# Optimization experiments

Hardware: AMD Instinct MI355X
Metric: run time of the kernel (lower is better)

The kernel has to match this reference:

```python
import jax, jax.numpy as jnp
from jax import lax
import numpy as np

T, B, P, A = 1000, 8192, 1024, 4
ER_DECAY = 1.0 - 1e-3  # per-trial exploration-rate decay


def setup_inputs() -> dict:
    key = jax.random.key(0)
    k1, k2, k3, k4 = jax.random.split(key, 4)
    params = jax.random.normal(k1, (13, P), dtype=jnp.float32) * 0.5
    choices = jax.random.randint(k2, (T, B), 0, A, dtype=jnp.int32)
    rewards = (jax.random.uniform(k3, (T, B)) < 0.5).astype(jnp.float32)
    pids = jax.random.randint(k4, (B,), 0, P, dtype=jnp.int32)
    return {"params": params, "rewards": rewards, "choices": choices, "pids": pids}


def _transform_params(params, pids):
    p = jnp.clip(params, -5.0, 5.0)
    sp, sg = jax.nn.softplus, jax.nn.sigmoid
    beta_r = jnp.clip(sp(p[0]), 0.01, 20.0)[pids]
    lapse = jnp.clip(sg(p[1]), 0.01, 0.99)[pids]
    prior = jnp.clip(sp(p[2]), 0.01, 0.99)[pids]
    alpha_er = jnp.clip(sg(p[3]), 0.01, 0.99)[pids]
    decay = jnp.clip(sg(p[4]), 0.01, 0.99)[pids]
    ab1 = p[5][pids]
    ab2 = p[6][pids]
    perv = sp(p[7])[pids]
    sw = p[8][pids]
    gam = sp(p[10])[pids]
    temp = jnp.clip(sp(p[11]) + 1e-6, 1e-6, 100.0)[pids]
    beta_p = sp(p[12])[pids]
    return beta_r, lapse, prior, alpha_er, decay, ab1, ab2, perv, sw, gam, temp, beta_p


def _forward(params, rewards, choices, pids):
    (beta_r, lapse, prior, alpha_er, decay, ab1, ab2,
     perv, sw, gam, temp, beta_p) = _transform_params(params, pids)
    nB = rewards.shape[1]

    q0 = prior[:, None] * jnp.ones((nB, A), dtype=rewards.dtype)
    carry0 = (q0,
              -jnp.ones((nB,), jnp.int32),          # old_choice
              jnp.zeros((nB,), rewards.dtype),       # trials since last switch
              alpha_er,                              # exploration rate
              jnp.zeros((nB, A), rewards.dtype))     # cumulative choice counts

    def step(carry, xs):
        q, old_choice, tsls, er, cum = carry
        choice, reward = xs                       # (B,), (B,)
        oh = jax.nn.one_hot(choice, A, dtype=q.dtype)        # (B, A)
        target = reward - gam * (1.0 - reward)                # loss-averse target
        q = q * (1.0 - oh) + oh * target[:, None]             # q[choice] = target
        same = choice == old_choice
        tsls = jnp.where(same, tsls + 1.0, 0.0)
        er = er * ER_DECAY
        cum = cum + oh
        # exploration smoothing toward mean, then decay
        q = (1.0 - er)[:, None] * q + er[:, None] * q.mean(-1, keepdims=True)
        q = q * decay[:, None]
        sm_in = beta_r[:, None] * q / temp[:, None] + beta_p[:, None] * jnp.log1p(cum)
        probs = (1.0 - lapse)[:, None] * jax.nn.softmax(sm_in, axis=-1) + lapse[:, None] / A
        cl = jnp.log(probs)
        samef = same.astype(q.dtype)[:, None]
        cl = (cl
              + samef * perv[:, None] * oh
              + (1.0 - samef) * sw[:, None] * oh
              + ab1[:, None] * jax.nn.one_hot(old_choice, A, dtype=q.dtype)  # old_choice=-1 -> zeros
              + ab2[:, None] * jax.nn.one_hot((choice + 2) % A, A, dtype=q.dtype)
              + oh * jnp.log(tsls + 1.0)[:, None])
        return (q, choice, tsls, er, cum), cl

    _, logits = lax.scan(step, carry0, (choices, rewards))
    return logits  # (T, B, A)


def reference(params, rewards, choices, pids):
    return _forward(params, rewards, choices, pids)
```

## Files before the change

### kernel.cpp

```cpp
#include <hip/hip_runtime.h>
#include <stdint.h>

#define T_TRIALS 1000
#define B_SIZE   8192
#define P_SIZE   1024
#define NGROUPS  125
#define ER_DECAY 0.999f
#define LN_ER_DECAY (-1.0005003335835335e-3f)
#define LOG2E_F 1.4426950408889634f
#define LN2_F   0.69314718055994531f

typedef float f32x4_t __attribute__((ext_vector_type(4)));

__device__ __forceinline__ float sp_(float x){ return __logf(1.0f + __expf(x)); }
__device__ __forceinline__ float sg_(float x){ return 1.0f / (1.0f + __expf(-x)); }
__device__ __forceinline__ float clampf(float x, float lo, float hi){ return fminf(fmaxf(x, lo), hi); }

template<int CHUNK_T, int KCH_T>
__global__ __launch_bounds__(256)
void castro_chunkmap_t(const float* __restrict__ params,
                       const float* __restrict__ rewards,
                       const int*   __restrict__ choices,
                       const int*   __restrict__ pids,
                       float4*      __restrict__ stageA,
                       uint32_t*    __restrict__ packed)
{
    constexpr int NM    = KCH_T - 1;
    constexpr int GRP_T = CHUNK_T / 8;
    constexpr int TAILG = (T_TRIALS - NM * CHUNK_T) / 8;

    const int b  = blockIdx.x * 256 + threadIdx.x;
    const int k  = blockIdx.y;
    const int t0 = k * CHUNK_T;

    const int*   cp = choices + (size_t)t0 * B_SIZE + b;
    const float* rp = rewards + (size_t)t0 * B_SIZE + b;
    uint32_t*    pk = packed + (size_t)(k * GRP_T) * B_SIZE + b;

    if (k == NM) {
        #pragma unroll
        for (int g = 0; g < GRP_T; ++g) {
            if (g < TAILG) {
                uint32_t gw = 0;
                #pragma unroll
                for (int i = 0; i < 8; ++i) {
                    const int   c = cp[(size_t)(g*8 + i) * B_SIZE];
                    const float r = rp[(size_t)(g*8 + i) * B_SIZE];
                    gw |= ((uint32_t)c | (r > 0.5f ? 4u : 0u)) << (4*i);
                }
                pk[(size_t)g * B_SIZE] = gw;
            }
        }
        return;
    }

    const int pid = pids[b];
    const float p3  = clampf(params[ 3 * P_SIZE + pid], -5.0f, 5.0f);
    const float p4  = clampf(params[ 4 * P_SIZE + pid], -5.0f, 5.0f);
    const float p10 = clampf(params[10 * P_SIZE + pid], -5.0f, 5.0f);
    const float alpha_er = clampf(sg_(p3), 0.01f, 0.99f);
    const float decay    = clampf(sg_(p4), 0.01f, 0.99f);
    const float gam      = sp_(p10);
    const float gp1      = 1.0f + gam;

    float er = alpha_er * __expf((float)t0 * LN_ER_DECAY);

    float m00=1.f,m01=0.f,m02=0.f,m03=0.f;
    float m10=0.f,m11=1.f,m12=0.f,m13=0.f;
    float m20=0.f,m21=0.f,m22=1.f,m23=0.f;
    float m30=0.f,m31=0.f,m32=0.f,m33=1.f;
    float b0=0.f,b1=0.f,b2=0.f,b3=0.f;
    int   c0=0,c1=0,c2=0,c3=0;
    int   run=0, last=-1;

    #pragma unroll
    for (int g = 0; g < GRP_T; ++g) {
        int cc[8]; float rr[8];
        #pragma unroll
        for (int i = 0; i < 8; ++i) {
            cc[i] = cp[(size_t)(g*8 + i) * B_SIZE];
            rr[i] = rp[(size_t)(g*8 + i) * B_SIZE];
        }
        uint32_t gw = 0;
        #pragma unroll
        for (int i = 0; i < 8; ++i) {
            const int   c = cc[i];
            const float r = rr[i];
            gw |= ((uint32_t)c | (r > 0.5f ? 4u : 0u)) << (4*i);

            er *= ER_DECAY;
            const float target = fmaf(r, gp1, -gam);
            const bool e0=(c==0), e1=(c==1), e2=(c==2), e3=(c==3);

            m00=e0?0.f:m00; m01=e0?0.f:m01; m02=e0?0.f:m02; m03=e0?0.f:m03; b0=e0?target:b0;
            m10=e1?0.f:m10; m11=e1?0.f:m11; m12=e1?0.f:m12; m13=e1?0.f:m13; b1=e1?target:b1;
            m20=e2?0.f:m20; m21=e2?0.f:m21; m22=e2?0.f:m22; m23=e2?0.f:m23; b2=e2?target:b2;
            m30=e3?0.f:m30; m31=e3?0.f:m31; m32=e3?0.f:m32; m33=e3?0.f:m33; b3=e3?target:b3;

            const float s0=(m00+m10)+(m20+m30);
            const float s1=(m01+m11)+(m21+m31);
            const float s2=(m02+m12)+(m22+m32);
            const float s3=(m03+m13)+(m23+m33);
            const float sb=(b0+b1)+(b2+b3);
            const float a  = decay * (1.0f - er);
            const float e4 = decay * er * 0.25f;

            m00=fmaf(e4,s0,a*m00); m01=fmaf(e4,s1,a*m01); m02=fmaf(e4,s2,a*m02); m03=fmaf(e4,s3,a*m03);
            m10=fmaf(e4,s0,a*m10); m11=fmaf(e4,s1,a*m11); m12=fmaf(e4,s2,a*m12); m13=fmaf(e4,s3,a*m13);
            m20=fmaf(e4,s0,a*m20); m21=fmaf(e4,s1,a*m21); m22=fmaf(e4,s2,a*m22); m23=fmaf(e4,s3,a*m23);
            m30=fmaf(e4,s0,a*m30); m31=fmaf(e4,s1,a*m31); m32=fmaf(e4,s2,a*m32); m33=fmaf(e4,s3,a*m33);
            b0=fmaf(e4,sb,a*b0); b1=fmaf(e4,sb,a*b1); b2=fmaf(e4,sb,a*b2); b3=fmaf(e4,sb,a*b3);

            c0 += e0; c1 += e1; c2 += e2; c3 += e3;
            run = (c == last) ? run + 1 : 1;
            last = c;
        }
        pk[(size_t)g * B_SIZE] = gw;
    }

    const size_t idx    = (size_t)k * B_SIZE + b;
    const size_t stride = (size_t)NM * B_SIZE;
    stageA[0*stride+idx] = make_float4(m00,m01,m02,m03);
    stageA[1*stride+idx] = make_float4(m10,m11,m12,m13);
    stageA[2*stride+idx] = make_float4(m20,m21,m22,m23);
    stageA[3*stride+idx] = make_float4(m30,m31,m32,m33);
    stageA[4*stride+idx] = make_float4(b0,b1,b2,b3);
    const unsigned meta0 = (unsigned)c0 | ((unsigned)c1<<8) | ((unsigned)c2<<16) | ((unsigned)c3<<24);
    const unsigned meta1 = (unsigned)last | ((unsigned)run<<8);
    stageA[5*stride+idx] = make_float4(__uint_as_float(meta0), __uint_as_float(meta1), 0.f, 0.f);
}

struct MapSet { float4 r0, r1, r2, r3, r4, r5; };
struct CombSt { float q0,q1,q2,q3; int n0,n1,n2,n3; int g_run, g_last; };

template<int NM>
__device__ __forceinline__ void load_set(MapSet& S, const float4* __restrict__ stageA, int kk, int b)
{
    const size_t stride = (size_t)NM * B_SIZE;
    const size_t i2 = (size_t)kk * B_SIZE + b;
    S.r0 = stageA[i2];          S.r1 = stageA[stride+i2];   S.r2 = stageA[2*stride+i2];
    S.r3 = stageA[3*stride+i2]; S.r4 = stageA[4*stride+i2]; S.r5 = stageA[5*stride+i2];
}

template<int CHUNK_T>
__device__ __forceinline__ void step_set(const MapSet& S, CombSt& st,
                                         float4* __restrict__ cpsA,
                                         float4* __restrict__ cpsB,
                                         float alpha_er, int kk, int b)
{
    const float nq0 = fmaf(S.r0.w,st.q3, fmaf(S.r0.z,st.q2, fmaf(S.r0.y,st.q1, fmaf(S.r0.x,st.q0, S.r4.x))));
    const float nq1 = fmaf(S.r1.w,st.q3, fmaf(S.r1.z,st.q2, fmaf(S.r1.y,st.q1, fmaf(S.r1.x,st.q0, S.r4.y))));
    const float nq2 = fmaf(S.r2.w,st.q3, fmaf(S.r2.z,st.q2, fmaf(S.r2.y,st.q1, fmaf(S.r2.x,st.q0, S.r4.z))));
    const float nq3 = fmaf(S.r3.w,st.q3, fmaf(S.r3.z,st.q2, fmaf(S.r3.y,st.q1, fmaf(S.r3.x,st.q0, S.r4.w))));
    st.q0=nq0; st.q1=nq1; st.q2=nq2; st.q3=nq3;

    const unsigned meta0 = __float_as_uint(S.r5.x);
    const unsigned meta1 = __float_as_uint(S.r5.y);
    st.n0 += (int)( meta0        & 255u);
    st.n1 += (int)((meta0 >> 8 ) & 255u);
    st.n2 += (int)((meta0 >> 16) & 255u);
    st.n3 += (int)( meta0 >> 24        );
    const int last = (int)(meta1 & 255u);
    const int rn   = (int)(meta1 >> 8);
    st.g_run  = (rn == CHUNK_T && last == st.g_last) ? st.g_run + CHUNK_T : rn;
    st.g_last = last;

    const float er_b = alpha_er * __expf((float)((kk+1)*CHUNK_T) * LN_ER_DECAY);
    const int   tsls = st.g_run - 1;

    const size_t ci = (size_t)kk * B_SIZE + b;
    cpsA[ci] = make_float4(st.q0,st.q1,st.q2,st.q3);
    cpsB[ci] = make_float4(er_b,
                           __uint_as_float((unsigned)st.n0 | ((unsigned)st.n1<<16)),
                           __uint_as_float((unsigned)st.n2 | ((unsigned)st.n3<<16)),
                           __uint_as_float((unsigned)tsls | ((unsigned)st.g_last<<16)));
}

template<int CHUNK_T, int KCH_T>
__global__ __launch_bounds__(64)
void castro_combine_t(const float* __restrict__ params,
                      const int*   __restrict__ pids,
                      const float4* __restrict__ stageA,
                      float4*      __restrict__ cpsA,
                      float4*      __restrict__ cpsB)
{
    constexpr int NM  = KCH_T - 1;
    constexpr int NM4 = ((NM + 3) / 4) * 4;

    const int b = blockIdx.x * 64 + threadIdx.x;
    const int pid = pids[b];
    const float p2 = clampf(params[2 * P_SIZE + pid], -5.0f, 5.0f);
    const float p3 = clampf(params[3 * P_SIZE + pid], -5.0f, 5.0f);
    const float prior    = clampf(sp_(p2), 0.01f, 0.99f);
    const float alpha_er = clampf(sg_(p3), 0.01f, 0.99f);

    CombSt st;
    st.q0=prior; st.q1=prior; st.q2=prior; st.q3=prior;
    st.n0=0; st.n1=0; st.n2=0; st.n3=0;
    st.g_run=0; st.g_last=-1;

    MapSet Am, Bm, Cm, Dm;
    load_set<NM>(Am, stageA, 0, b);
    load_set<NM>(Bm, stageA, 1, b);
    load_set<NM>(Cm, stageA, 2, b);
    load_set<NM>(Dm, stageA, 3, b);

    #pragma unroll
    for (int k0 = 0; k0 < NM4; k0 += 4) {
        if (k0   < NM) { step_set<CHUNK_T>(Am, st, cpsA, cpsB, alpha_er, k0,   b); if (k0+4 < NM) load_set<NM>(Am, stageA, k0+4, b); }
        if (k0+1 < NM) { step_set<CHUNK_T>(Bm, st, cpsA, cpsB, alpha_er, k0+1, b); if (k0+5 < NM) load_set<NM>(Bm, stageA, k0+5, b); }
        if (k0+2 < NM) { step_set<CHUNK_T>(Cm, st, cpsA, cpsB, alpha_er, k0+2, b); if (k0+6 < NM) load_set<NM>(Cm, stageA, k0+6, b); }
        if (k0+3 < NM) { step_set<CHUNK_T>(Dm, st, cpsA, cpsB, alpha_er, k0+3, b); if (k0+7 < NM) load_set<NM>(Dm, stageA, k0+7, b); }
    }
}

template<int CHUNK_T, int KCH_T>
__global__ __launch_bounds__(256)
void castro_emit_t(const float* __restrict__ params,
                   const int*   __restrict__ pids,
                   const float4* __restrict__ cpsA,
                   const float4* __restrict__ cpsB,
                   const uint32_t* __restrict__ packed,
                   float4*      __restrict__ out4)
{
    constexpr int GRP_T = CHUNK_T / 8;
    constexpr int TAILG = (T_TRIALS - (KCH_T-1) * CHUNK_T) / 8;

    const int b  = blockIdx.x * 256 + threadIdx.x;
    const int k  = blockIdx.y;
    const int t0 = k * CHUNK_T;
    const int ngroups = (k == KCH_T-1) ? TAILG : GRP_T;
    const int pid = pids[b];

    float p[13];
    #pragma unroll
    for (int kk = 0; kk < 13; ++kk)
        p[kk] = clampf(params[kk * P_SIZE + pid], -5.0f, 5.0f);

    const float beta_r   = clampf(sp_(p[0]), 0.01f, 20.0f);
    const float lapse    = clampf(sg_(p[1]), 0.01f, 0.99f);
    const float prior    = clampf(sp_(p[2]), 0.01f, 0.99f);
    const float alpha_er = clampf(sg_(p[3]), 0.01f, 0.99f);
    const float decay    = clampf(sg_(p[4]), 0.01f, 0.99f);
    const float ab1      = p[5];
    const float ab2      = p[6];
    const float perv     = sp_(p[7]);
    const float sw       = p[8];
    const float gam      = sp_(p[10]);
    const float temp     = clampf(sp_(p[11]) + 1e-6f, 1e-6f, 100.0f);
    const float beta_p   = sp_(p[12]);

    const float bt2 = (beta_r / temp) * LOG2E_F;
    const float ol  = 1.0f - lapse;
    const float la4 = 0.25f * lapse;
    const float gp1 = 1.0f + gam;

    float q0,q1,q2,q3, er, ft;
    float f0,f1,f2,f3;
    int   old_c;
    if (k == 0) {
        q0=q1=q2=q3=prior; f0=f1=f2=f3=0.f; ft=-1.f; old_c=-1; er=alpha_er;
        ft = 0.f;
    } else {
        const size_t ci = (size_t)(k-1) * B_SIZE + b;
        const float4 s0 = cpsA[ci];
        const float4 s1 = cpsB[ci];
        q0=s0.x; q1=s0.y; q2=s0.z; q3=s0.w;
        er = s1.x;
        const unsigned u1=__float_as_uint(s1.y), u2=__float_as_uint(s1.z), u3=__float_as_uint(s1.w);
        f0=(float)(int)(u1&0xFFFFu); f1=(float)(int)(u1>>16);
        f2=(float)(int)(u2&0xFFFFu); f3=(float)(int)(u2>>16);
        ft=(float)(int)(u3&0xFFFFu); old_c=(int)(u3>>16);
    }
    float bpl0 = beta_p * __log2f(1.0f + f0);
    float bpl1 = beta_p * __log2f(1.0f + f1);
    float bpl2 = beta_p * __log2f(1.0f + f2);
    float bpl3 = beta_p * __log2f(1.0f + f3);

    const uint32_t* pk = packed + (size_t)(k * GRP_T) * B_SIZE + b;
    float4* op = out4 + (size_t)t0 * B_SIZE + b;

    #pragma unroll
    for (int g = 0; g < GRP_T; ++g) {
        if (g < ngroups) {
            const uint32_t w = pk[(size_t)g * B_SIZE];
            #pragma unroll
            for (int i = 0; i < 8; ++i) {
                const int   code = (int)((w >> (4*i)) & 0xFu);
                const int   c    = code & 3;
                const float r    = (float)((code >> 2) & 1);

                const float target = fmaf(r, gp1, -gam);
                const bool e0=(c==0), e1=(c==1), e2=(c==2), e3=(c==3);
                q0 = e0 ? target : q0;
                q1 = e1 ? target : q1;
                q2 = e2 ? target : q2;
                q3 = e3 ? target : q3;

                const bool same = (c == old_c);
                ft = same ? ft + 1.0f : 0.0f;
                er *= ER_DECAY;

                const float fsel = e0 ? f0 : (e1 ? f1 : (e2 ? f2 : f3));
                const float bplc = beta_p * __log2f(fsel + 2.0f);
                f0 += e0 ? 1.0f : 0.0f;
                f1 += e1 ? 1.0f : 0.0f;
                f2 += e2 ? 1.0f : 0.0f;
                f3 += e3 ? 1.0f : 0.0f;
                bpl0 = e0 ? bplc : bpl0;
                bpl1 = e1 ? bplc : bpl1;
                bpl2 = e2 ? bplc : bpl2;
                bpl3 = e3 ? bplc : bpl3;

                const float qm = 0.25f * ((q0+q1)+(q2+q3));
                q0 = decay * fmaf(er, qm - q0, q0);
                q1 = decay * fmaf(er, qm - q1, q1);
                q2 = decay * fmaf(er, qm - q2, q2);
                q3 = decay * fmaf(er, qm - q3, q3);

                const float s0 = fmaf(bt2, q0, bpl0);
                const float s1 = fmaf(bt2, q1, bpl1);
                const float s2 = fmaf(bt2, q2, bpl2);
                const float s3 = fmaf(bt2, q3, bpl3);

                const float m  = fmaxf(fmaxf(s0, s1), fmaxf(s2, s3));
                const float x0 = exp2f(s0 - m);
                const float x1 = exp2f(s1 - m);
                const float x2 = exp2f(s2 - m);
                const float x3 = exp2f(s3 - m);
                const float inv = __builtin_amdgcn_rcpf((x0+x1)+(x2+x3));
                const float sc  = ol * inv;

                const float L0 = __log2f(fmaf(sc, x0, la4));
                const float L1 = __log2f(fmaf(sc, x1, la4));
                const float L2 = __log2f(fmaf(sc, x2, la4));
                const float L3 = __log2f(fmaf(sc, x3, la4));

                const float bonus = fmaf(LN2_F, __log2f(ft + 1.0f), same ? perv : sw);

                float a0 = (e0 ? bonus : 0.0f) + ((old_c == 0) ? ab1 : 0.0f);
                float a1 = (e1 ? bonus : 0.0f) + ((old_c == 1) ? ab1 : 0.0f);
                float a2 = (e2 ? bonus : 0.0f) + ((old_c == 2) ? ab1 : 0.0f);
                float a3 = (e3 ? bonus : 0.0f) + ((old_c == 3) ? ab1 : 0.0f);
                const int c2 = (c + 2) & 3;
                a0 += (c2 == 0) ? ab2 : 0.0f;
                a1 += (c2 == 1) ? ab2 : 0.0f;
                a2 += (c2 == 2) ? ab2 : 0.0f;
                a3 += (c2 == 3) ? ab2 : 0.0f;

                f32x4_t v = { fmaf(LN2_F, L0, a0), fmaf(LN2_F, L1, a1),
                              fmaf(LN2_F, L2, a2), fmaf(LN2_F, L3, a3) };
                __builtin_nontemporal_store(v, reinterpret_cast<f32x4_t*>(op + (size_t)(g*8 + i) * B_SIZE));
                old_c = c;
            }
        }
    }
}

__global__ __launch_bounds__(64)
void castro_scan(const float* __restrict__ params,
                 const float* __restrict__ rewards,
                 const int*   __restrict__ choices,
                 const int*   __restrict__ pids,
                 float*       __restrict__ out)
{
    const int b = blockIdx.x * blockDim.x + threadIdx.x;
    if (b >= B_SIZE) return;
    const int pid = pids[b];
    float p[13];
    #pragma unroll
    for (int kk = 0; kk < 13; ++kk)
        p[kk] = clampf(params[kk * P_SIZE + pid], -5.0f, 5.0f);
    const float beta_r   = clampf(sp_(p[0]), 0.01f, 20.0f);
    const float lapse    = clampf(sg_(p[1]), 0.01f, 0.99f);
    const float prior    = clampf(sp_(p[2]), 0.01f, 0.99f);
    const float alpha_er = clampf(sg_(p[3]), 0.01f, 0.99f);
    const float decay    = clampf(sg_(p[4]), 0.01f, 0.99f);
    const float ab1 = p[5], ab2 = p[6];
    const float perv = sp_(p[7]), sw = p[8];
    const float gam  = sp_(p[10]);
    const float temp = clampf(sp_(p[11]) + 1e-6f, 1e-6f, 100.0f);
    const float beta_p = sp_(p[12]);
    const float bt = beta_r / temp, ol = 1.0f - lapse, la4 = 0.25f * lapse, gp1 = 1.0f + gam;

    float q0=prior,q1=prior,q2=prior,q3=prior;
    float n0=0,n1=0,n2=0,n3=0;
    int old_c=-1; float tsls=0.0f, er=alpha_er;
    const int* cp = choices + b;
    const float* rp = rewards + b;
    float4* op = reinterpret_cast<float4*>(out) + b;
    for (int t = 0; t < T_TRIALS; ++t) {
        const int c = cp[(size_t)t*B_SIZE];
        const float r = rp[(size_t)t*B_SIZE];
        const float target = fmaf(r, gp1, -gam);
        const bool e0=(c==0),e1=(c==1),e2=(c==2),e3=(c==3);
        q0=e0?target:q0; q1=e1?target:q1; q2=e2?target:q2; q3=e3?target:q3;
        const bool same = (c == old_c);
        tsls = same ? tsls + 1.0f : 0.0f;
        er *= ER_DECAY;
        n0+=e0?1.f:0.f; n1+=e1?1.f:0.f; n2+=e2?1.f:0.f; n3+=e3?1.f:0.f;
        const float qm = 0.25f*((q0+q1)+(q2+q3));
        q0 = decay*fmaf(er, qm-q0, q0); q1 = decay*fmaf(er, qm-q1, q1);
        q2 = decay*fmaf(er, qm-q2, q2); q3 = decay*fmaf(er, qm-q3, q3);
        float s0 = fmaf(bt,q0,beta_p*__logf(1.f+n0));
        float s1 = fmaf(bt,q1,beta_p*__logf(1.f+n1));
        float s2 = fmaf(bt,q2,beta_p*__logf(1.f+n2));
        float s3 = fmaf(bt,q3,beta_p*__logf(1.f+n3));
        const float m = fmaxf(fmaxf(s0,s1),fmaxf(s2,s3));
        const float x0=__expf(s0-m),x1=__expf(s1-m),x2=__expf(s2-m),x3=__expf(s3-m);
        const float inv=__builtin_amdgcn_rcpf((x0+x1)+(x2+x3));
        const float sc=ol*inv;
        float l0=__logf(fmaf(sc,x0,la4)), l1=__logf(fmaf(sc,x1,la4));
        float l2=__logf(fmaf(sc,x2,la4)), l3=__logf(fmaf(sc,x3,la4));
        const float bonus=(same?perv:sw)+__logf(tsls+1.0f);
        l0+=e0?bonus:0.f; l1+=e1?bonus:0.f; l2+=e2?bonus:0.f; l3+=e3?bonus:0.f;
        l0+=(old_c==0)?ab1:0.f; l1+=(old_c==1)?ab1:0.f; l2+=(old_c==2)?ab1:0.f; l3+=(old_c==3)?ab1:0.f;
        const int c2=(c+2)&3;
        l0+=(c2==0)?ab2:0.f; l1+=(c2==1)?ab2:0.f; l2+=(c2==2)?ab2:0.f; l3+=(c2==3)?ab2:0.f;
        op[(size_t)t*B_SIZE] = make_float4(l0,l1,l2,l3);
        old_c=c;
    }
}

template<int CHUNK_T, int KCH_T>
static void launch_pipeline(const float* params, const float* rewards,
                            const int* choices, const int* pids,
                            void* d_out, void* d_ws, hipStream_t stream)
{
    constexpr int NM = KCH_T - 1;
    float4*   stageA = (float4*)d_ws;
    float4*   cpsA   = stageA + (size_t)6 * NM * B_SIZE;
    float4*   cpsB   = cpsA + (size_t)NM * B_SIZE;
    uint32_t* packed = (uint32_t*)(cpsB + (size_t)NM * B_SIZE);

    hipLaunchKernelGGL(HIP_KERNEL_NAME(castro_chunkmap_t<CHUNK_T, KCH_T>),
                       dim3(B_SIZE/256, KCH_T), dim3(256), 0, stream,
                       params, rewards, choices, pids, stageA, packed);
    hipLaunchKernelGGL(HIP_KERNEL_NAME(castro_combine_t<CHUNK_T, KCH_T>),
                       dim3(B_SIZE/64), dim3(64), 0, stream,
                       params, pids, stageA, cpsA, cpsB);
    hipLaunchKernelGGL(HIP_KERNEL_NAME(castro_emit_t<CHUNK_T, KCH_T>),
                       dim3(B_SIZE/256, KCH_T), dim3(256), 0, stream,
                       params, pids, cpsA, cpsB, packed, (float4*)d_out);
}

extern "C" void kernel_launch(void* const* d_in, const int* in_sizes, int n_in,
                              void* d_out, int out_size, void* d_ws, size_t ws_size,
                              hipStream_t stream)
{
    const float* params  = (const float*)d_in[0];
    const float* rewards = (const float*)d_in[1];
    const int*   choices = (const int*)  d_in[2];
    const int*   pids    = (const int*)  d_in[3];

    const size_t need32 = (size_t)31 * B_SIZE * 128 + (size_t)NGROUPS * B_SIZE * 4;
    const size_t need40 = (size_t)24 * B_SIZE * 128 + (size_t)NGROUPS * B_SIZE * 4;

    if (ws_size >= need32) {
        launch_pipeline<32, 32>(params, rewards, choices, pids, d_out, d_ws, stream);
    } else if (ws_size >= need40) {
        launch_pipeline<40, 25>(params, rewards, choices, pids, d_out, d_ws, stream);
    } else {
        hipLaunchKernelGGL(castro_scan, dim3(B_SIZE/64), dim3(64), 0, stream,
                           params, rewards, choices, pids, (float*)d_out);
    }
}
```

Before: 69.54 us.

## Decouple map chunk size from emit chunk size with replay from checkpoints

The map stage now builds 9 long 104-trial affine maps instead of 31 short ones, while the emit stage keeps 32-trial chunks. Each emit block replays the scalar recurrence from the nearest map checkpoint using the packed choice/reward words before it writes outputs. This shortens the serial combine chain and shrinks the stageA workspace, at the cost of redundant replay work in emit (up to about 96 trials per thread). It also software-prefetches the next 8-trial group of inputs in the map kernel and replaces the nontemporal output stores with ordinary stores.

Result: slower. 90.83 us (+30.6%).

```diff
diff --git a/kernel.cpp b/kernel.cpp
--- a/kernel.cpp
+++ b/kernel.cpp
@@ -4,52 +4,47 @@
 #define T_TRIALS 1000
 #define B_SIZE   8192
 #define P_SIZE   1024
-#define NGROUPS  125
+#define MAPC     104
+#define NMAP     9
+#define EMITC    32
+#define KEMIT    32
+#define NWORDS   125
 #define ER_DECAY 0.999f
 #define LN_ER_DECAY (-1.0005003335835335e-3f)
 #define LOG2E_F 1.4426950408889634f
 #define LN2_F   0.69314718055994531f
 
-typedef float f32x4_t __attribute__((ext_vector_type(4)));
-
 __device__ __forceinline__ float sp_(float x){ return __logf(1.0f + __expf(x)); }
 __device__ __forceinline__ float sg_(float x){ return 1.0f / (1.0f + __expf(-x)); }
 __device__ __forceinline__ float clampf(float x, float lo, float hi){ return fminf(fmaxf(x, lo), hi); }
 
-template<int CHUNK_T, int KCH_T>
 __global__ __launch_bounds__(256)
-void castro_chunkmap_t(const float* __restrict__ params,
-                       const float* __restrict__ rewards,
-                       const int*   __restrict__ choices,
-                       const int*   __restrict__ pids,
-                       float4*      __restrict__ stageA,
-                       uint32_t*    __restrict__ packed)
-{
-    constexpr int NM    = KCH_T - 1;
-    constexpr int GRP_T = CHUNK_T / 8;
-    constexpr int TAILG = (T_TRIALS - NM * CHUNK_T) / 8;
-
+void castro_mappack(const float* __restrict__ params,
+                    const float* __restrict__ rewards,
+                    const int*   __restrict__ choices,
+                    const int*   __restrict__ pids,
+                    float4*      __restrict__ stageA,
+                    uint32_t*    __restrict__ packed)
+{
     const int b  = blockIdx.x * 256 + threadIdx.x;
-    const int k  = blockIdx.y;
-    const int t0 = k * CHUNK_T;
+    const int j  = blockIdx.y;
+    const int t0 = j * MAPC;
 
     const int*   cp = choices + (size_t)t0 * B_SIZE + b;
     const float* rp = rewards + (size_t)t0 * B_SIZE + b;
-    uint32_t*    pk = packed + (size_t)(k * GRP_T) * B_SIZE + b;
-
-    if (k == NM) {
+
+    if (j == NMAP) {
+        uint32_t* pk = packed + (size_t)(NMAP * 13) * B_SIZE + b;
         #pragma unroll
-        for (int g = 0; g < GRP_T; ++g) {
-            if (g < TAILG) {
-                uint32_t gw = 0;
-                #pragma unroll
-                for (int i = 0; i < 8; ++i) {
-                    const int   c = cp[(size_t)(g*8 + i) * B_SIZE];
-                    const float r = rp[(size_t)(g*8 + i) * B_SIZE];
-                    gw |= ((uint32_t)c | (r > 0.5f ? 4u : 0u)) << (4*i);
-                }
-                pk[(size_t)g * B_SIZE] = gw;
+        for (int g = 0; g < 8; ++g) {
+            uint32_t gw = 0;
+            #pragma unroll
+            for (int i = 0; i < 8; ++i) {
+                const int   c = cp[(size_t)(g*8 + i) * B_SIZE];
+                const float r = rp[(size_t)(g*8 + i) * B_SIZE];
+                gw |= ((uint32_t)c | (r > 0.5f ? 4u : 0u)) << (4*i);
             }
+            pk[(size_t)g * B_SIZE] = gw;
         }
         return;
     }
@@ -73,13 +68,23 @@
     int   c0=0,c1=0,c2=0,c3=0;
     int   run=0, last=-1;
 
-    #pragma unroll
-    for (int g = 0; g < GRP_T; ++g) {
+    uint32_t* pk = packed + (size_t)(j * 13) * B_SIZE + b;
+
+    int   cbuf[8]; float rbuf[8];
+    #pragma unroll
+    for (int i = 0; i < 8; ++i) { cbuf[i] = cp[(size_t)i * B_SIZE]; rbuf[i] = rp[(size_t)i * B_SIZE]; }
+
+    #pragma unroll
+    for (int g = 0; g < 13; ++g) {
         int cc[8]; float rr[8];
         #pragma unroll
-        for (int i = 0; i < 8; ++i) {
-            cc[i] = cp[(size_t)(g*8 + i) * B_SIZE];
-            rr[i] = rp[(size_t)(g*8 + i) * B_SIZE];
+        for (int i = 0; i < 8; ++i) { cc[i] = cbuf[i]; rr[i] = rbuf[i]; }
+        if (g < 12) {
+            #pragma unroll
+            for (int i = 0; i < 8; ++i) {
+                cbuf[i] = cp[(size_t)((g+1)*8 + i) * B_SIZE];
+                rbuf[i] = rp[(size_t)((g+1)*8 + i) * B_SIZE];
+            }
         }
         uint32_t gw = 0;
         #pragma unroll
@@ -118,8 +123,8 @@
         pk[(size_t)g * B_SIZE] = gw;
     }
 
-    const size_t idx    = (size_t)k * B_SIZE + b;
-    const size_t stride = (size_t)NM * B_SIZE;
+    const size_t idx    = (size_t)j * B_SIZE + b;
+    const size_t stride = (size_t)NMAP * B_SIZE;
     stageA[0*stride+idx] = make_float4(m00,m01,m02,m03);
     stageA[1*stride+idx] = make_float4(m10,m11,m12,m13);
     stageA[2*stride+idx] = make_float4(m20,m21,m22,m23);
@@ -133,16 +138,14 @@
 struct MapSet { float4 r0, r1, r2, r3, r4, r5; };
 struct CombSt { float q0,q1,q2,q3; int n0,n1,n2,n3; int g_run, g_last; };
 
-template<int NM>
 __device__ __forceinline__ void load_set(MapSet& S, const float4* __restrict__ stageA, int kk, int b)
 {
-    const size_t stride = (size_t)NM * B_SIZE;
+    const size_t stride = (size_t)NMAP * B_SIZE;
     const size_t i2 = (size_t)kk * B_SIZE + b;
     S.r0 = stageA[i2];          S.r1 = stageA[stride+i2];   S.r2 = stageA[2*stride+i2];
     S.r3 = stageA[3*stride+i2]; S.r4 = stageA[4*stride+i2]; S.r5 = stageA[5*stride+i2];
 }
 
-template<int CHUNK_T>
 __device__ __forceinline__ void step_set(const MapSet& S, CombSt& st,
                                          float4* __restrict__ cpsA,
                                          float4* __restrict__ cpsB,
@@ -162,10 +165,10 @@
     st.n3 += (int)( meta0 >> 24        );
     const int last = (int)(meta1 & 255u);
     const int rn   = (int)(meta1 >> 8);
-    st.g_run  = (rn == CHUNK_T && last == st.g_last) ? st.g_run + CHUNK_T : rn;
+    st.g_run  = (rn == MAPC && last == st.g_last) ? st.g_run + MAPC : rn;
     st.g_last = last;
 
-    const float er_b = alpha_er * __expf((float)((kk+1)*CHUNK_T) * LN_ER_DECAY);
+    const float er_b = alpha_er * __expf((float)((kk+1)*MAPC) * LN_ER_DECAY);
     const int   tsls = st.g_run - 1;
 
     const size_t ci = (size_t)kk * B_SIZE + b;
@@ -176,17 +179,13 @@
                            __uint_as_float((unsigned)tsls | ((unsigned)st.g_last<<16)));
 }
 
-template<int CHUNK_T, int KCH_T>
 __global__ __launch_bounds__(64)
-void castro_combine_t(const float* __restrict__ params,
-                      const int*   __restrict__ pids,
-                      const float4* __restrict__ stageA,
-                      float4*      __restrict__ cpsA,
-                      float4*      __restrict__ cpsB)
-{
-    constexpr int NM  = KCH_T - 1;
-    constexpr int NM4 = ((NM + 3) / 4) * 4;
-
+void castro_combine2(const float* __restrict__ params,
+                     const int*   __restrict__ pids,
+                     const float4* __restrict__ stageA,
+                     float4*      __restrict__ cpsA,
+                     float4*      __restrict__ cpsB)
+{
     const int b = blockIdx.x * 64 + threadIdx.x;
     const int pid = pids[b];
     const float p2 = clampf(params[2 * P_SIZE + pid], -5.0f, 5.0f);
@@ -200,36 +199,32 @@
     st.g_run=0; st.g_last=-1;
 
     MapSet Am, Bm, Cm, Dm;
-    load_set<NM>(Am, stageA, 0, b);
-    load_set<NM>(Bm, stageA, 1, b);
-    load_set<NM>(Cm, stageA, 2, b);
-    load_set<NM>(Dm, stageA, 3, b);
-
-    #pragma unroll
-    for (int k0 = 0; k0 < NM4; k0 += 4) {
-        if (k0   < NM) { step_set<CHUNK_T>(Am, st, cpsA, cpsB, alpha_er, k0,   b); if (k0+4 < NM) load_set<NM>(Am, stageA, k0+4, b); }
-        if (k0+1 < NM) { step_set<CHUNK_T>(Bm, st, cpsA, cpsB, alpha_er, k0+1, b); if (k0+5 < NM) load_set<NM>(Bm, stageA, k0+5, b); }
-        if (k0+2 < NM) { step_set<CHUNK_T>(Cm, st, cpsA, cpsB, alpha_er, k0+2, b); if (k0+6 < NM) load_set<NM>(Cm, stageA, k0+6, b); }
-        if (k0+3 < NM) { step_set<CHUNK_T>(Dm, st, cpsA, cpsB, alpha_er, k0+3, b); if (k0+7 < NM) load_set<NM>(Dm, stageA, k0+7, b); }
-    }
-}
-
-template<int CHUNK_T, int KCH_T>
+    load_set(Am, stageA, 0, b);
+    load_set(Bm, stageA, 1, b);
+    load_set(Cm, stageA, 2, b);
+    load_set(Dm, stageA, 3, b);
+
+    #pragma unroll
+    for (int k0 = 0; k0 < 12; k0 += 4) {
+        if (k0   < NMAP) { step_set(Am, st, cpsA, cpsB, alpha_er, k0,   b); if (k0+4 < NMAP) load_set(Am, stageA, k0+4, b); }
+        if (k0+1 < NMAP) { step_set(Bm, st, cpsA, cpsB, alpha_er, k0+1, b); if (k0+5 < NMAP) load_set(Bm, stageA, k0+5, b); }
+        if (k0+2 < NMAP) { step_set(Cm, st, cpsA, cpsB, alpha_er, k0+2, b); if (k0+6 < NMAP) load_set(Cm, stageA, k0+6, b); }
+        if (k0+3 < NMAP) { step_set(Dm, st, cpsA, cpsB, alpha_er, k0+3, b); if (k0+7 < NMAP) load_set(Dm, stageA, k0+7, b); }
+    }
+}
+
 __global__ __launch_bounds__(256)
-void castro_emit_t(const float* __restrict__ params,
-                   const int*   __restrict__ pids,
-                   const float4* __restrict__ cpsA,
-                   const float4* __restrict__ cpsB,
-                   const uint32_t* __restrict__ packed,
-                   float4*      __restrict__ out4)
-{
-    constexpr int GRP_T = CHUNK_T / 8;
-    constexpr int TAILG = (T_TRIALS - (KCH_T-1) * CHUNK_T) / 8;
-
+void castro_emit2(const float* __restrict__ params,
+                  const int*   __restrict__ pids,
+                  const float4* __restrict__ cpsA,
+                  const float4* __restrict__ cpsB,
+                  const uint32_t* __restrict__ packed,
+                  float4*      __restrict__ out4)
+{
     const int b  = blockIdx.x * 256 + threadIdx.x;
     const int k  = blockIdx.y;
-    const int t0 = k * CHUNK_T;
-    const int ngroups = (k == KCH_T-1) ? TAILG : GRP_T;
+    const int t0 = k * EMITC;
+    const int ngroups = (k == KEMIT-1) ? (T_TRIALS - (KEMIT-1)*EMITC)/8 : EMITC/8;
     const int pid = pids[b];
 
     float p[13];
@@ -258,11 +253,11 @@
     float q0,q1,q2,q3, er, ft;
     float f0,f1,f2,f3;
     int   old_c;
-    if (k == 0) {
-        q0=q1=q2=q3=prior; f0=f1=f2=f3=0.f; ft=-1.f; old_c=-1; er=alpha_er;
-        ft = 0.f;
+    const int j_cp = t0 / MAPC;
+    if (j_cp == 0) {
+        q0=q1=q2=q3=prior; f0=f1=f2=f3=0.f; ft=0.f; old_c=-1; er=alpha_er;
     } else {
-        const size_t ci = (size_t)(k-1) * B_SIZE + b;
+        const size_t ci = (size_t)(j_cp-1) * B_SIZE + b;
         const float4 s0 = cpsA[ci];
         const float4 s1 = cpsB[ci];
         q0=s0.x; q1=s0.y; q2=s0.z; q3=s0.w;
@@ -272,21 +267,54 @@
         f2=(float)(int)(u2&0xFFFFu); f3=(float)(int)(u2>>16);
         ft=(float)(int)(u3&0xFFFFu); old_c=(int)(u3>>16);
     }
+
+    const uint32_t* pkr = packed + b;
+
+    const int tstart = j_cp * MAPC;
+    const int nw = (t0 - tstart) >> 3;
+    for (int w = 0; w < nw; ++w) {
+        uint32_t word = pkr[(size_t)((tstart >> 3) + w) * B_SIZE];
+        #pragma unroll
+        for (int i = 0; i < 8; ++i) {
+            const int   code = (int)(word & 0xFu); word >>= 4;
+            const int   c    = code & 3;
+            const float r    = (float)((code >> 2) & 1);
+            const float target = fmaf(r, gp1, -gam);
+            const bool e0=(c==0), e1=(c==1), e2=(c==2), e3=(c==3);
+            q0 = e0 ? target : q0;
+            q1 = e1 ? target : q1;
+            q2 = e2 ? target : q2;
+            q3 = e3 ? target : q3;
+            const bool same = (c == old_c);
+            ft = same ? ft + 1.0f : 0.0f;
+            er *= ER_DECAY;
+            f0 += e0 ? 1.0f : 0.0f;
+            f1 += e1 ? 1.0f : 0.0f;
+            f2 += e2 ? 1.0f : 0.0f;
+            f3 += e3 ? 1.0f : 0.0f;
+            const float qm = 0.25f * ((q0+q1)+(q2+q3));
+            q0 = decay * fmaf(er, qm - q0, q0);
+            q1 = decay * fmaf(er, qm - q1, q1);
+            q2 = decay * fmaf(er, qm - q2, q2);
+            q3 = decay * fmaf(er, qm - q3, q3);
+            old_c = c;
+        }
+    }
+
     float bpl0 = beta_p * __log2f(1.0f + f0);
     float bpl1 = beta_p * __log2f(1.0f + f1);
     float bpl2 = beta_p * __log2f(1.0f + f2);
     float bpl3 = beta_p * __log2f(1.0f + f3);
 
-    const uint32_t* pk = packed + (size_t)(k * GRP_T) * B_SIZE + b;
     float4* op = out4 + (size_t)t0 * B_SIZE + b;
 
     #pragma unroll
-    for (int g = 0; g < GRP_T; ++g) {
+    for (int g = 0; g < EMITC/8; ++g) {
         if (g < ngroups) {
-            const uint32_t w = pk[(size_t)g * B_SIZE];
+            uint32_t word = pkr[(size_t)((t0 >> 3) + g) * B_SIZE];
             #pragma unroll
             for (int i = 0; i < 8; ++i) {
-                const int   code = (int)((w >> (4*i)) & 0xFu);
+                const int   code = (int)(word & 0xFu); word >>= 4;
                 const int   c    = code & 3;
                 const float r    = (float)((code >> 2) & 1);
 
@@ -348,9 +376,9 @@
                 a2 += (c2 == 2) ? ab2 : 0.0f;
                 a3 += (c2 == 3) ? ab2 : 0.0f;
 
-                f32x4_t v = { fmaf(LN2_F, L0, a0), fmaf(LN2_F, L1, a1),
-                              fmaf(LN2_F, L2, a2), fmaf(LN2_F, L3, a3) };
-                __builtin_nontemporal_store(v, reinterpret_cast<f32x4_t*>(op + (size_t)(g*8 + i) * B_SIZE));
+                op[(size_t)(g*8 + i) * B_SIZE] =
+                    make_float4(fmaf(LN2_F, L0, a0), fmaf(LN2_F, L1, a1),
+                                fmaf(LN2_F, L2, a2), fmaf(LN2_F, L3, a3));
                 old_c = c;
             }
         }
@@ -422,28 +450,6 @@
     }
 }
 
-template<int CHUNK_T, int KCH_T>
-static void launch_pipeline(const float* params, const float* rewards,
-                            const int* choices, const int* pids,
-                            void* d_out, void* d_ws, hipStream_t stream)
-{
-    constexpr int NM = KCH_T - 1;
-    float4*   stageA = (float4*)d_ws;
-    float4*   cpsA   = stageA + (size_t)6 * NM * B_SIZE;
-    float4*   cpsB   = cpsA + (size_t)NM * B_SIZE;
-    uint32_t* packed = (uint32_t*)(cpsB + (size_t)NM * B_SIZE);
-
-    hipLaunchKernelGGL(HIP_KERNEL_NAME(castro_chunkmap_t<CHUNK_T, KCH_T>),
-                       dim3(B_SIZE/256, KCH_T), dim3(256), 0, stream,
-                       params, rewards, choices, pids, stageA, packed);
-    hipLaunchKernelGGL(HIP_KERNEL_NAME(castro_combine_t<CHUNK_T, KCH_T>),
-                       dim3(B_SIZE/64), dim3(64), 0, stream,
-                       params, pids, stageA, cpsA, cpsB);
-    hipLaunchKernelGGL(HIP_KERNEL_NAME(castro_emit_t<CHUNK_T, KCH_T>),
-                       dim3(B_SIZE/256, KCH_T), dim3(256), 0, stream,
-                       params, pids, cpsA, cpsB, packed, (float4*)d_out);
-}
-
 extern "C" void kernel_launch(void* const* d_in, const int* in_sizes, int n_in,
                               void* d_out, int out_size, void* d_ws, size_t ws_size,
                               hipStream_t stream)
@@ -453,15 +459,25 @@
     const int*   choices = (const int*)  d_in[2];
     const int*   pids    = (const int*)  d_in[3];
 
-    const size_t need32 = (size_t)31 * B_SIZE * 128 + (size_t)NGROUPS * B_SIZE * 4;
-    const size_t need40 = (size_t)24 * B_SIZE * 128 + (size_t)NGROUPS * B_SIZE * 4;
-
-    if (ws_size >= need32) {
-        launch_pipeline<32, 32>(params, rewards, choices, pids, d_out, d_ws, stream);
-    } else if (ws_size >= need40) {
-        launch_pipeline<40, 25>(params, rewards, choices, pids, d_out, d_ws, stream);
-    } else {
-        hipLaunchKernelGGL(castro_scan, dim3(B_SIZE/64), dim3(64), 0, stream,
-                           params, rewards, choices, pids, (float*)d_out);
-    }
-}
+    const size_t need = (size_t)NMAP * B_SIZE * 96
+                      + (size_t)NMAP * B_SIZE * 32
+                      + (size_t)NWORDS * B_SIZE * 4;
+
+    if (ws_size >= need) {
+        float4*   stageA = (float4*)d_ws;
+        float4*   cpsA   = stageA + (size_t)6 * NMAP * B_SIZE;
+        float4*   cpsB   = cpsA + (size_t)NMAP * B_SIZE;
+        uint32_t* packed = (uint32_t*)(cpsB + (size_t)NMAP * B_SIZE);
+
+        hipLaunchKernelGGL(castro_mappack, dim3(B_SIZE/256, NMAP+1), dim3(256), 0, stream,
+                           params, rewards, choices, pids, stageA, packed);
+        hipLaunchKernelGGL(castro_combine2, dim3(B_SIZE/64), dim3(64), 0, stream,
+                           params, pids, stageA, cpsA, cpsB);
+        hipLaunchKernelGGL(castro_emit2, dim3(B_SIZE/256, KEMIT), dim3(256), 0, stream,
+                           params, pids, cpsA, cpsB, packed, (float4*)d_out);
+        return;
+    }
+
+    hipLaunchKernelGGL(castro_scan, dim3(B_SIZE/64), dim3(64), 0, stream,
+                       params, rewards, choices, pids, (float*)d_out);
+}
```

## Replace serial chunk combine with warp-parallel Hillis-Steele scan over affine maps

Applied to the files above, without the earlier changes.

The combine kernel used to walk 31 chunk maps one after another in a single thread per batch element. It now assigns 32 lanes per batch element and runs a log-step shuffle scan that composes the 4x4 affine maps, choice counts and run-length state. The goal is to cut the serial latency of the middle stage and raise its parallelism. In exchange each step does a full 4x4 matrix product and about 27 shuffles, far more arithmetic overall. The templated CHUNK/KCH variants are hardcoded to 32, and the 40-chunk fallback is removed.

After: 73.07 us. 5.1% more time.

```diff
diff --git a/kernel.cpp b/kernel.cpp
--- a/kernel.cpp
+++ b/kernel.cpp
@@ -4,7 +4,10 @@
 #define T_TRIALS 1000
 #define B_SIZE   8192
 #define P_SIZE   1024
-#define NGROUPS  125
+#define CHUNK    32
+#define KCH      32
+#define NM       31
+#define NWORDS   125
 #define ER_DECAY 0.999f
 #define LN_ER_DECAY (-1.0005003335835335e-3f)
 #define LOG2E_F 1.4426950408889634f
@@ -16,41 +19,31 @@
 __device__ __forceinline__ float sg_(float x){ return 1.0f / (1.0f + __expf(-x)); }
 __device__ __forceinline__ float clampf(float x, float lo, float hi){ return fminf(fmaxf(x, lo), hi); }
 
-template<int CHUNK_T, int KCH_T>
 __global__ __launch_bounds__(256)
-void castro_chunkmap_t(const float* __restrict__ params,
-                       const float* __restrict__ rewards,
-                       const int*   __restrict__ choices,
-                       const int*   __restrict__ pids,
-                       float4*      __restrict__ stageA,
-                       uint32_t*    __restrict__ packed)
+void castro_chunkmap(const float* __restrict__ params,
+                     const float* __restrict__ rewards,
+                     const int*   __restrict__ choices,
+                     const int*   __restrict__ pids,
+                     float4*      __restrict__ stageA,
+                     uint32_t*    __restrict__ packed)
 {
-    constexpr int NM    = KCH_T - 1;
-    constexpr int GRP_T = CHUNK_T / 8;
-    constexpr int TAILG = (T_TRIALS - NM * CHUNK_T) / 8;
-
     const int b  = blockIdx.x * 256 + threadIdx.x;
     const int k  = blockIdx.y;
-    const int t0 = k * CHUNK_T;
+    const int t0 = k * CHUNK;
 
     const int*   cp = choices + (size_t)t0 * B_SIZE + b;
     const float* rp = rewards + (size_t)t0 * B_SIZE + b;
-    uint32_t*    pk = packed + (size_t)(k * GRP_T) * B_SIZE + b;
+    uint32_t*    pk = packed + (size_t)(k * 4) * B_SIZE + b;
 
     if (k == NM) {
-        #pragma unroll
-        for (int g = 0; g < GRP_T; ++g) {
-            if (g < TAILG) {
-                uint32_t gw = 0;
-                #pragma unroll
-                for (int i = 0; i < 8; ++i) {
-                    const int   c = cp[(size_t)(g*8 + i) * B_SIZE];
-                    const float r = rp[(size_t)(g*8 + i) * B_SIZE];
-                    gw |= ((uint32_t)c | (r > 0.5f ? 4u : 0u)) << (4*i);
-                }
-                pk[(size_t)g * B_SIZE] = gw;
-            }
+        uint32_t gw = 0;
+        #pragma unroll
+        for (int i = 0; i < 8; ++i) {
+            const int   c = cp[(size_t)i * B_SIZE];
+            const float r = rp[(size_t)i * B_SIZE];
+            gw |= ((uint32_t)c | (r > 0.5f ? 4u : 0u)) << (4*i);
         }
+        pk[0] = gw;
         return;
     }
 
@@ -74,7 +67,7 @@
     int   run=0, last=-1;
 
     #pragma unroll
-    for (int g = 0; g < GRP_T; ++g) {
+    for (int g = 0; g < 4; ++g) {
         int cc[8]; float rr[8];
         #pragma unroll
         for (int i = 0; i < 8; ++i) {
@@ -125,111 +118,143 @@
     stageA[2*stride+idx] = make_float4(m20,m21,m22,m23);
     stageA[3*stride+idx] = make_float4(m30,m31,m32,m33);
     stageA[4*stride+idx] = make_float4(b0,b1,b2,b3);
-    const unsigned meta0 = (unsigned)c0 | ((unsigned)c1<<8) | ((unsigned)c2<<16) | ((unsigned)c3<<24);
-    const unsigned meta1 = (unsigned)last | ((unsigned)run<<8);
-    stageA[5*stride+idx] = make_float4(__uint_as_float(meta0), __uint_as_float(meta1), 0.f, 0.f);
+    const int meta0 = c0 | (c1<<8) | (c2<<16) | (c3<<24);
+    const int meta1 = last | (run<<8);
+    stageA[5*stride+idx] = make_float4(__int_as_float(meta0), __int_as_float(meta1), 0.f, 0.f);
 }
 
-struct MapSet { float4 r0, r1, r2, r3, r4, r5; };
-struct CombSt { float q0,q1,q2,q3; int n0,n1,n2,n3; int g_run, g_last; };
-
-template<int NM>
-__device__ __forceinline__ void load_set(MapSet& S, const float4* __restrict__ stageA, int kk, int b)
-{
-    const size_t stride = (size_t)NM * B_SIZE;
-    const size_t i2 = (size_t)kk * B_SIZE + b;
-    S.r0 = stageA[i2];          S.r1 = stageA[stride+i2];   S.r2 = stageA[2*stride+i2];
-    S.r3 = stageA[3*stride+i2]; S.r4 = stageA[4*stride+i2]; S.r5 = stageA[5*stride+i2];
-}
-
-template<int CHUNK_T>
-__device__ __forceinline__ void step_set(const MapSet& S, CombSt& st,
-                                         float4* __restrict__ cpsA,
-                                         float4* __restrict__ cpsB,
-                                         float alpha_er, int kk, int b)
-{
-    const float nq0 = fmaf(S.r0.w,st.q3, fmaf(S.r0.z,st.q2, fmaf(S.r0.y,st.q1, fmaf(S.r0.x,st.q0, S.r4.x))));
-    const float nq1 = fmaf(S.r1.w,st.q3, fmaf(S.r1.z,st.q2, fmaf(S.r1.y,st.q1, fmaf(S.r1.x,st.q0, S.r4.y))));
-    const float nq2 = fmaf(S.r2.w,st.q3, fmaf(S.r2.z,st.q2, fmaf(S.r2.y,st.q1, fmaf(S.r2.x,st.q0, S.r4.z))));
-    const float nq3 = fmaf(S.r3.w,st.q3, fmaf(S.r3.z,st.q2, fmaf(S.r3.y,st.q1, fmaf(S.r3.x,st.q0, S.r4.w))));
-    st.q0=nq0; st.q1=nq1; st.q2=nq2; st.q3=nq3;
-
-    const unsigned meta0 = __float_as_uint(S.r5.x);
-    const unsigned meta1 = __float_as_uint(S.r5.y);
-    st.n0 += (int)( meta0        & 255u);
-    st.n1 += (int)((meta0 >> 8 ) & 255u);
-    st.n2 += (int)((meta0 >> 16) & 255u);
-    st.n3 += (int)( meta0 >> 24        );
-    const int last = (int)(meta1 & 255u);
-    const int rn   = (int)(meta1 >> 8);
-    st.g_run  = (rn == CHUNK_T && last == st.g_last) ? st.g_run + CHUNK_T : rn;
-    st.g_last = last;
-
-    const float er_b = alpha_er * __expf((float)((kk+1)*CHUNK_T) * LN_ER_DECAY);
-    const int   tsls = st.g_run - 1;
-
-    const size_t ci = (size_t)kk * B_SIZE + b;
-    cpsA[ci] = make_float4(st.q0,st.q1,st.q2,st.q3);
-    cpsB[ci] = make_float4(er_b,
-                           __uint_as_float((unsigned)st.n0 | ((unsigned)st.n1<<16)),
-                           __uint_as_float((unsigned)st.n2 | ((unsigned)st.n3<<16)),
-                           __uint_as_float((unsigned)tsls | ((unsigned)st.g_last<<16)));
-}
-
-template<int CHUNK_T, int KCH_T>
-__global__ __launch_bounds__(64)
-void castro_combine_t(const float* __restrict__ params,
+__global__ __launch_bounds__(256)
+void castro_combine_w(const float* __restrict__ params,
                       const int*   __restrict__ pids,
                       const float4* __restrict__ stageA,
                       float4*      __restrict__ cpsA,
                       float4*      __restrict__ cpsB)
 {
-    constexpr int NM  = KCH_T - 1;
-    constexpr int NM4 = ((NM + 3) / 4) * 4;
-
-    const int b = blockIdx.x * 64 + threadIdx.x;
+    const int tid = threadIdx.x;
+    const int k   = tid & 31;
+    const int b   = blockIdx.x * 8 + (tid >> 5);
+
     const int pid = pids[b];
     const float p2 = clampf(params[2 * P_SIZE + pid], -5.0f, 5.0f);
     const float p3 = clampf(params[3 * P_SIZE + pid], -5.0f, 5.0f);
     const float prior    = clampf(sp_(p2), 0.01f, 0.99f);
     const float alpha_er = clampf(sg_(p3), 0.01f, 0.99f);
 
-    CombSt st;
-    st.q0=prior; st.q1=prior; st.q2=prior; st.q3=prior;
-    st.n0=0; st.n1=0; st.n2=0; st.n3=0;
-    st.g_run=0; st.g_last=-1;
-
-    MapSet Am, Bm, Cm, Dm;
-    load_set<NM>(Am, stageA, 0, b);
-    load_set<NM>(Bm, stageA, 1, b);
-    load_set<NM>(Cm, stageA, 2, b);
-    load_set<NM>(Dm, stageA, 3, b);
+    float M[16], bv[4];
+    int   cn[4], run, last, len;
+
+    if (k < NM) {
+        const size_t stride = (size_t)NM * B_SIZE;
+        const size_t i2 = (size_t)k * B_SIZE + b;
+        const float4 r0 = stageA[i2];
+        const float4 r1 = stageA[stride + i2];
+        const float4 r2 = stageA[2*stride + i2];
+        const float4 r3 = stageA[3*stride + i2];
+        const float4 r4 = stageA[4*stride + i2];
+        const float4 r5 = stageA[5*stride + i2];
+        M[0]=r0.x; M[1]=r0.y; M[2]=r0.z;  M[3]=r0.w;
+        M[4]=r1.x; M[5]=r1.y; M[6]=r1.z;  M[7]=r1.w;
+        M[8]=r2.x; M[9]=r2.y; M[10]=r2.z; M[11]=r2.w;
+        M[12]=r3.x; M[13]=r3.y; M[14]=r3.z; M[15]=r3.w;
+        bv[0]=r4.x; bv[1]=r4.y; bv[2]=r4.z; bv[3]=r4.w;
+        const int meta0 = __float_as_int(r5.x);
+        const int meta1 = __float_as_int(r5.y);
+        cn[0] =  meta0        & 255;
+        cn[1] = (meta0 >> 8 ) & 255;
+        cn[2] = (meta0 >> 16) & 255;
+        cn[3] = (meta0 >> 24) & 255;
+        last = meta1 & 255;
+        run  = meta1 >> 8;
+        len  = CHUNK;
+    } else {
+        #pragma unroll
+        for (int i = 0; i < 16; ++i) M[i] = (i % 5 == 0) ? 1.0f : 0.0f;
+        bv[0]=bv[1]=bv[2]=bv[3]=0.f;
+        cn[0]=cn[1]=cn[2]=cn[3]=0;
+        run=0; last=-1; len=0;
+    }
 
     #pragma unroll
-    for (int k0 = 0; k0 < NM4; k0 += 4) {
-        if (k0   < NM) { step_set<CHUNK_T>(Am, st, cpsA, cpsB, alpha_er, k0,   b); if (k0+4 < NM) load_set<NM>(Am, stageA, k0+4, b); }
-        if (k0+1 < NM) { step_set<CHUNK_T>(Bm, st, cpsA, cpsB, alpha_er, k0+1, b); if (k0+5 < NM) load_set<NM>(Bm, stageA, k0+5, b); }
-        if (k0+2 < NM) { step_set<CHUNK_T>(Cm, st, cpsA, cpsB, alpha_er, k0+2, b); if (k0+6 < NM) load_set<NM>(Cm, stageA, k0+6, b); }
-        if (k0+3 < NM) { step_set<CHUNK_T>(Dm, st, cpsA, cpsB, alpha_er, k0+3, b); if (k0+7 < NM) load_set<NM>(Dm, stageA, k0+7, b); }
+    for (int o = 1; o < 32; o <<= 1) {
+        float xM[16], xb[4];
+        int   xc[4], xrun, xlast, xlen;
+        #pragma unroll
+        for (int i = 0; i < 16; ++i) xM[i] = __shfl_up(M[i], (unsigned)o, 32);
+        #pragma unroll
+        for (int i = 0; i < 4; ++i)  xb[i] = __shfl_up(bv[i], (unsigned)o, 32);
+        #pragma unroll
+        for (int i = 0; i < 4; ++i)  xc[i] = __shfl_up(cn[i], (unsigned)o, 32);
+        xrun  = __shfl_up(run,  (unsigned)o, 32);
+        xlast = __shfl_up(last, (unsigned)o, 32);
+        xlen  = __shfl_up(len,  (unsigned)o, 32);
+
+        const bool v = (k >= o);
+        #pragma unroll
+        for (int i = 0; i < 16; ++i) xM[i] = v ? xM[i] : ((i % 5 == 0) ? 1.0f : 0.0f);
+        #pragma unroll
+        for (int i = 0; i < 4; ++i)  xb[i] = v ? xb[i] : 0.0f;
+        #pragma unroll
+        for (int i = 0; i < 4; ++i)  xc[i] = v ? xc[i] : 0;
+        xrun  = v ? xrun  : 0;
+        xlast = v ? xlast : -1;
+        xlen  = v ? xlen  : 0;
+
+        float nM[16], nb[4];
+        #pragma unroll
+        for (int r = 0; r < 4; ++r) {
+            #pragma unroll
+            for (int c = 0; c < 4; ++c) {
+                nM[r*4+c] = fmaf(M[r*4+0], xM[0*4+c],
+                             fmaf(M[r*4+1], xM[1*4+c],
+                              fmaf(M[r*4+2], xM[2*4+c],
+                                   M[r*4+3]* xM[3*4+c])));
+            }
+            nb[r] = fmaf(M[r*4+0], xb[0],
+                     fmaf(M[r*4+1], xb[1],
+                      fmaf(M[r*4+2], xb[2],
+                       fmaf(M[r*4+3], xb[3], bv[r]))));
+        }
+        #pragma unroll
+        for (int i = 0; i < 16; ++i) M[i] = nM[i];
+        #pragma unroll
+        for (int i = 0; i < 4; ++i)  bv[i] = nb[i];
+        #pragma unroll
+        for (int i = 0; i < 4; ++i)  cn[i] += xc[i];
+
+        run = (run == len && last == xlast) ? xrun + run : run;
+        len += xlen;
+    }
+
+    if (k < NM) {
+        const float q0 = fmaf(prior, (M[0] +M[1]) +(M[2] +M[3]),  bv[0]);
+        const float q1 = fmaf(prior, (M[4] +M[5]) +(M[6] +M[7]),  bv[1]);
+        const float q2 = fmaf(prior, (M[8] +M[9]) +(M[10]+M[11]), bv[2]);
+        const float q3 = fmaf(prior, (M[12]+M[13])+(M[14]+M[15]), bv[3]);
+
+        const float er_b = alpha_er * __expf((float)((k+1)*CHUNK) * LN_ER_DECAY);
+        const int   tsls = run - 1;
+
+        const size_t ci = (size_t)k * B_SIZE + b;
+        cpsA[ci] = make_float4(q0, q1, q2, q3);
+        cpsB[ci] = make_float4(er_b,
+                               __int_as_float(cn[0] | (cn[1]<<16)),
+                               __int_as_float(cn[2] | (cn[3]<<16)),
+                               __int_as_float((tsls & 0xFFFF) | (last<<16)));
     }
 }
 
-template<int CHUNK_T, int KCH_T>
 __global__ __launch_bounds__(256)
-void castro_emit_t(const float* __restrict__ params,
-                   const int*   __restrict__ pids,
-                   const float4* __restrict__ cpsA,
-                   const float4* __restrict__ cpsB,
-                   const uint32_t* __restrict__ packed,
-                   float4*      __restrict__ out4)
+void castro_emit(const float* __restrict__ params,
+                 const int*   __restrict__ pids,
+                 const float4* __restrict__ cpsA,
+                 const float4* __restrict__ cpsB,
+                 const uint32_t* __restrict__ packed,
+                 float4*      __restrict__ out4)
 {
-    constexpr int GRP_T = CHUNK_T / 8;
-    constexpr int TAILG = (T_TRIALS - (KCH_T-1) * CHUNK_T) / 8;
-
     const int b  = blockIdx.x * 256 + threadIdx.x;
     const int k  = blockIdx.y;
-    const int t0 = k * CHUNK_T;
-    const int ngroups = (k == KCH_T-1) ? TAILG : GRP_T;
+    const int t0 = k * CHUNK;
+    const int ngroups = (k == KCH-1) ? 1 : 4;
     const int pid = pids[b];
 
     float p[13];
@@ -259,34 +284,34 @@
     float f0,f1,f2,f3;
     int   old_c;
     if (k == 0) {
-        q0=q1=q2=q3=prior; f0=f1=f2=f3=0.f; ft=-1.f; old_c=-1; er=alpha_er;
-        ft = 0.f;
+        q0=q1=q2=q3=prior; f0=f1=f2=f3=0.f; ft=0.f; old_c=-1; er=alpha_er;
     } else {
         const size_t ci = (size_t)(k-1) * B_SIZE + b;
         const float4 s0 = cpsA[ci];
         const float4 s1 = cpsB[ci];
         q0=s0.x; q1=s0.y; q2=s0.z; q3=s0.w;
         er = s1.x;
-        const unsigned u1=__float_as_uint(s1.y), u2=__float_as_uint(s1.z), u3=__float_as_uint(s1.w);
-        f0=(float)(int)(u1&0xFFFFu); f1=(float)(int)(u1>>16);
-        f2=(float)(int)(u2&0xFFFFu); f3=(float)(int)(u2>>16);
-        ft=(float)(int)(u3&0xFFFFu); old_c=(int)(u3>>16);
-    }
+        const int u1=__float_as_int(s1.y), u2=__float_as_int(s1.z), u3=__float_as_int(s1.w);
+        f0=(float)(u1&0xFFFF); f1=(float)(u1>>16);
+        f2=(float)(u2&0xFFFF); f3=(float)(u2>>16);
+        ft=(float)(u3&0xFFFF); old_c=(u3>>16);
+    }
+
     float bpl0 = beta_p * __log2f(1.0f + f0);
     float bpl1 = beta_p * __log2f(1.0f + f1);
     float bpl2 = beta_p * __log2f(1.0f + f2);
     float bpl3 = beta_p * __log2f(1.0f + f3);
 
-    const uint32_t* pk = packed + (size_t)(k * GRP_T) * B_SIZE + b;
+    const uint32_t* pk = packed + (size_t)(k * 4) * B_SIZE + b;
     float4* op = out4 + (size_t)t0 * B_SIZE + b;
 
     #pragma unroll
-    for (int g = 0; g < GRP_T; ++g) {
+    for (int g = 0; g < 4; ++g) {
         if (g < ngroups) {
-            const uint32_t w = pk[(size_t)g * B_SIZE];
+            uint32_t word = pk[(size_t)g * B_SIZE];
             #pragma unroll
             for (int i = 0; i < 8; ++i) {
-                const int   code = (int)((w >> (4*i)) & 0xFu);
+                const int   code = (int)(word & 0xFu); word >>= 4;
                 const int   c    = code & 3;
                 const float r    = (float)((code >> 2) & 1);
 
@@ -350,7 +375,8 @@
 
                 f32x4_t v = { fmaf(LN2_F, L0, a0), fmaf(LN2_F, L1, a1),
                               fmaf(LN2_F, L2, a2), fmaf(LN2_F, L3, a3) };
-                __builtin_nontemporal_store(v, reinterpret_cast<f32x4_t*>(op + (size_t)(g*8 + i) * B_SIZE));
+                __builtin_nontemporal_store(v,
+                    reinterpret_cast<f32x4_t*>(op + (size_t)(g*8 + i) * B_SIZE));
                 old_c = c;
             }
         }
@@ -422,28 +448,6 @@
     }
 }
 
-template<int CHUNK_T, int KCH_T>
-static void launch_pipeline(const float* params, const float* rewards,
-                            const int* choices, const int* pids,
-                            void* d_out, void* d_ws, hipStream_t stream)
-{
-    constexpr int NM = KCH_T - 1;
-    float4*   stageA = (float4*)d_ws;
-    float4*   cpsA   = stageA + (size_t)6 * NM * B_SIZE;
-    float4*   cpsB   = cpsA + (size_t)NM * B_SIZE;
-    uint32_t* packed = (uint32_t*)(cpsB + (size_t)NM * B_SIZE);
-
-    hipLaunchKernelGGL(HIP_KERNEL_NAME(castro_chunkmap_t<CHUNK_T, KCH_T>),
-                       dim3(B_SIZE/256, KCH_T), dim3(256), 0, stream,
-                       params, rewards, choices, pids, stageA, packed);
-    hipLaunchKernelGGL(HIP_KERNEL_NAME(castro_combine_t<CHUNK_T, KCH_T>),
-                       dim3(B_SIZE/64), dim3(64), 0, stream,
-                       params, pids, stageA, cpsA, cpsB);
-    hipLaunchKernelGGL(HIP_KERNEL_NAME(castro_emit_t<CHUNK_T, KCH_T>),
-                       dim3(B_SIZE/256, KCH_T), dim3(256), 0, stream,
-                       params, pids, cpsA, cpsB, packed, (float4*)d_out);
-}
-
 extern "C" void kernel_launch(void* const* d_in, const int* in_sizes, int n_in,
                               void* d_out, int out_size, void* d_ws, size_t ws_size,
                               hipStream_t stream)
@@ -453,15 +457,25 @@
     const int*   choices = (const int*)  d_in[2];
     const int*   pids    = (const int*)  d_in[3];
 
-    const size_t need32 = (size_t)31 * B_SIZE * 128 + (size_t)NGROUPS * B_SIZE * 4;
-    const size_t need40 = (size_t)24 * B_SIZE * 128 + (size_t)NGROUPS * B_SIZE * 4;
-
-    if (ws_size >= need32) {
-        launch_pipeline<32, 32>(params, rewards, choices, pids, d_out, d_ws, stream);
-    } else if (ws_size >= need40) {
-        launch_pipeline<40, 25>(params, rewards, choices, pids, d_out, d_ws, stream);
-    } else {
-        hipLaunchKernelGGL(castro_scan, dim3(B_SIZE/64), dim3(64), 0, stream,
-                           params, rewards, choices, pids, (float*)d_out);
-    }
+    const size_t need = (size_t)NM * B_SIZE * 96
+                      + (size_t)NM * B_SIZE * 32
+                      + (size_t)NWORDS * B_SIZE * 4;
+
+    if (ws_size >= need) {
+        float4*   stageA = (float4*)d_ws;
+        float4*   cpsA   = stageA + (size_t)6 * NM * B_SIZE;
+        float4*   cpsB   = cpsA + (size_t)NM * B_SIZE;
+        uint32_t* packed = (uint32_t*)(cpsB + (size_t)NM * B_SIZE);
+
+        hipLaunchKernelGGL(castro_chunkmap, dim3(B_SIZE/256, KCH), dim3(256), 0, stream,
+                           params, rewards, choices, pids, stageA, packed);
+        hipLaunchKernelGGL(castro_combine_w, dim3(B_SIZE/8), dim3(256), 0, stream,
+                           params, pids, stageA, cpsA, cpsB);
+        hipLaunchKernelGGL(castro_emit, dim3(B_SIZE/256, KCH), dim3(256), 0, stream,
+                           params, pids, cpsA, cpsB, packed, (float4*)d_out);
+        return;
+    }
+
+    hipLaunchKernelGGL(castro_scan, dim3(B_SIZE/64), dim3(64), 0, stream,
+                       params, rewards, choices, pids, (float*)d_out);
 }
```
